# Kernel tuning notes

Hardware: AMD Instinct MI355X
Metric: run time of the kernel (lower is better)

Reference implementation:

```python
import jax, jax.numpy as jnp
import numpy as np

DIM = 768
H = 12  # num_heads -> head width W = 64 (required by internal reshapes)


def setup_inputs() -> dict:
    key = jax.random.key(0)
    ks = jax.random.split(key, 16)
    B, S = 1, 128  # V = Q = A = 128 tokens
    d = {
        "v": jax.random.normal(ks[0], (B, S, DIM), jnp.float32),
        "q": jax.random.normal(ks[1], (B, S, DIM), jnp.float32),
        "a": jax.random.normal(ks[2], (B, S, DIM), jnp.float32),
        "v_mask": jnp.ones((B, S), jnp.bool_),  # unused by the module, kept for signature parity
        "q_mask": jnp.ones((B, S), jnp.bool_),
        "a_mask": jnp.ones((B, S), jnp.bool_),
    }
    scale = 0.02
    names = ["Wv", "Wq", "Wa", "Wvo", "Wqo", "Wao"]
    for i, n in enumerate(names):
        d[n] = jax.random.normal(ks[3 + i], (DIM, DIM), jnp.float32) * scale
        d["b" + n[1:].lower()] = jnp.zeros((DIM,), jnp.float32)
    return d


def _heads(x):
    # (B, S, D) -> (B, H, S, W)
    B, S, D = x.shape
    return x.reshape(B, S, H, D // H).transpose(0, 2, 1, 3)


def reference(v, q, a, v_mask, q_mask, a_mask,
              Wv, bv, Wq, bq, Wa, ba, Wvo, bvo, Wqo, bqo, Wao, bao):
    B, Sv, D = v.shape
    Sq, Sa = q.shape[1], a.shape[1]
    W = D // H
    nv, nq, na = Sv // 8, Sq // 8, Sa // 8

    # first projections (masks are unused in the original forward)
    vp = v @ Wv + bv
    qp = q @ Wq + bq
    ap = a @ Wa + ba
    # output projections are applied to the ALREADY-projected tensors (as in source)
    vo = vp @ Wvo + bvo
    qo = qp @ Wqo + bqo
    ao = ap @ Wao + bao

    vh, qh, ah = _heads(vp), _heads(qp), _heads(ap)          # (B,H,S,W)
    voh, qoh, aoh = _heads(vo), _heads(qo), _heads(ao)

    # trilinear scores: (B,H,V,Q,A)
    att = jnp.einsum('bhvw,bhqw,bhaw->bhvqa', vh, qh, ah) / jnp.sqrt(jnp.asarray(W, vh.dtype))
    K = nv * nq * na
    # faithful to source: view(-1, H, nv*nq*na) then softmax over last axis, view back
    att = jax.nn.softmax(att.reshape(-1, H, K), axis=-1)
    att = att.reshape(-1, H, nv, nq, na)  # dropout p=0 -> identity
    B2 = att.shape[0]

    # source uses att.size(2) (= nv) for ALL three reshapes (requires V=Q=A)
    vor = voh.reshape(B2, H, nv, -1)
    qor = qoh.reshape(B2, H, nv, -1)
    aor = aoh.reshape(B2, H, nv, -1)

    v_out = jnp.einsum('bhvqa,bhvw->bvhw', att, vor).reshape(-1, DIM)
    q_out = jnp.einsum('bhvqa,bhqw->bqhw', att, qor).reshape(-1, DIM)
    a_out = jnp.einsum('bhvqa,bhaw->bahw', att, aor).reshape(-1, DIM)
    return (v_out, q_out, a_out)
```

## Files before the change

### kernel.cpp

```cpp
#include <hip/hip_runtime.h>


#define DIM   768
#define SEQ   128
#define NH    12
#define HW    64
#define PROJ_ELEMS (SEQ * DIM)
#define QOUT_OFF   98304
#define AOUT_OFF   196608

typedef _Float16 f16x8 __attribute__((ext_vector_type(8)));
typedef float    f32x4 __attribute__((ext_vector_type(4)));

__global__ __launch_bounds__(64) void proj_kernel(
    const void* __restrict__ A0, const void* __restrict__ A1, const void* __restrict__ A2,
    const float* __restrict__ W0, const float* __restrict__ W1, const float* __restrict__ W2,
    const float* __restrict__ b0, const float* __restrict__ b1, const float* __restrict__ b2,
    void* __restrict__ C0, void* __restrict__ C1, void* __restrict__ C2,
    int a_f16, int out_f16)
{
    const int mat = blockIdx.z;
    const void* __restrict__ A   = (mat == 0) ? A0 : (mat == 1) ? A1 : A2;
    const float* __restrict__ W  = (mat == 0) ? W0 : (mat == 1) ? W1 : W2;
    const float* __restrict__ bb = (mat == 0) ? b0 : (mat == 1) ? b1 : b2;
    void* __restrict__ C         = (mat == 0) ? C0 : (mat == 1) ? C1 : C2;

    const int m0   = blockIdx.x * 16;
    const int n0   = blockIdx.y * 16;
    const int lane = threadIdx.x & 63;
    const int fm   = lane & 15;
    const int fk   = (lane >> 4) << 3;

    const float* __restrict__ pw = W + fk * DIM + n0 + fm;

    f32x4 acc = (f32x4){0.f, 0.f, 0.f, 0.f};

    if (a_f16) {
        const _Float16* __restrict__ pa = (const _Float16*)A + (m0 + fm) * DIM + fk;
        #pragma unroll
        for (int s = 0; s < 24; ++s) {
            const f16x8 af = *(const f16x8*)(pa + 32 * s);
            const float* __restrict__ w = pw + 32 * s * DIM;
            float w0 = w[0 * DIM], w1 = w[1 * DIM], w2 = w[2 * DIM], w3 = w[3 * DIM];
            float w4 = w[4 * DIM], w5 = w[5 * DIM], w6 = w[6 * DIM], w7 = w[7 * DIM];
            f16x8 wf;
            wf[0] = (_Float16)w0; wf[1] = (_Float16)w1;
            wf[2] = (_Float16)w2; wf[3] = (_Float16)w3;
            wf[4] = (_Float16)w4; wf[5] = (_Float16)w5;
            wf[6] = (_Float16)w6; wf[7] = (_Float16)w7;
            acc = __builtin_amdgcn_mfma_f32_16x16x32_f16(af, wf, acc, 0, 0, 0);
        }
    } else {
        const float* __restrict__ pa = (const float*)A + (m0 + fm) * DIM + fk;
        #pragma unroll
        for (int s = 0; s < 24; ++s) {
            const f32x4 alo = *(const f32x4*)(pa + 32 * s);
            const f32x4 ahi = *(const f32x4*)(pa + 32 * s + 4);
            f16x8 af;
            af[0] = (_Float16)alo[0]; af[1] = (_Float16)alo[1];
            af[2] = (_Float16)alo[2]; af[3] = (_Float16)alo[3];
            af[4] = (_Float16)ahi[0]; af[5] = (_Float16)ahi[1];
            af[6] = (_Float16)ahi[2]; af[7] = (_Float16)ahi[3];
            const float* __restrict__ w = pw + 32 * s * DIM;
            float w0 = w[0 * DIM], w1 = w[1 * DIM], w2 = w[2 * DIM], w3 = w[3 * DIM];
            float w4 = w[4 * DIM], w5 = w[5 * DIM], w6 = w[6 * DIM], w7 = w[7 * DIM];
            f16x8 wf;
            wf[0] = (_Float16)w0; wf[1] = (_Float16)w1;
            wf[2] = (_Float16)w2; wf[3] = (_Float16)w3;
            wf[4] = (_Float16)w4; wf[5] = (_Float16)w5;
            wf[6] = (_Float16)w6; wf[7] = (_Float16)w7;
            acc = __builtin_amdgcn_mfma_f32_16x16x32_f16(af, wf, acc, 0, 0, 0);
        }
    }

    const int col  = n0 + fm;
    const int row0 = m0 + ((lane >> 4) << 2);
    const float bi = bb[col];
    #pragma unroll
    for (int rr = 0; rr < 4; ++rr) {
        const float val = acc[rr] + bi;
        if (out_f16) ((_Float16*)C)[(row0 + rr) * DIM + col] = (_Float16)val;
        else         ((float*)C)[(row0 + rr) * DIM + col]    = val;
    }
}

__global__ __launch_bounds__(256) void fused_attn_kernel(
    const _Float16* __restrict__ vpH, const _Float16* __restrict__ qpH,
    const _Float16* __restrict__ apH,
    const float* __restrict__ vo, const float* __restrict__ qo, const float* __restrict__ ao,
    float* __restrict__ out)
{
    const int vtok = blockIdx.x;
    const int h    = blockIdx.y;

    __shared__ _Float16 vqL[128][72];
    __shared__ _Float16 ahL[128][72];

    const int t    = threadIdx.x;
    const int w    = t >> 6;
    const int lane = t & 63;
    const int fm   = lane & 15;
    const int fk   = (lane >> 4) << 3;

    {
        const int r  = t >> 1;
        const int kh = (t & 1) << 5;
        const _Float16* pq = qpH + r    * DIM + h * HW + kh;
        const _Float16* pv = vpH + vtok * DIM + h * HW + kh;
        const _Float16* pa = apH + r    * DIM + h * HW + kh;
        #pragma unroll
        for (int u = 0; u < 4; ++u) {
            const f16x8 qv = *(const f16x8*)(pq + 8 * u);
            const f16x8 vv = *(const f16x8*)(pv + 8 * u);
            const f16x8 av = *(const f16x8*)(pa + 8 * u);
            *(f16x8*)&vqL[r][kh + 8 * u] = qv * vv;
            *(f16x8*)&ahL[r][kh + 8 * u] = av;
        }
    }
    __syncthreads();

    f32x4 acc[2][8];
    #pragma unroll
    for (int qt = 0; qt < 2; ++qt)
        #pragma unroll
        for (int at = 0; at < 8; ++at)
            acc[qt][at] = (f32x4){0.f, 0.f, 0.f, 0.f};

    const int q0 = 32 * w;
    #pragma unroll
    for (int ks = 0; ks < 2; ++ks) {
        const f16x8 af0 = *(const f16x8*)&vqL[q0 + fm     ][32 * ks + fk];
        const f16x8 af1 = *(const f16x8*)&vqL[q0 + 16 + fm][32 * ks + fk];
        #pragma unroll
        for (int at = 0; at < 8; ++at) {
            const f16x8 bf = *(const f16x8*)&ahL[16 * at + fm][32 * ks + fk];
            acc[0][at] = __builtin_amdgcn_mfma_f32_16x16x32_f16(af0, bf, acc[0][at], 0, 0, 0);
            acc[1][at] = __builtin_amdgcn_mfma_f32_16x16x32_f16(af1, bf, acc[1][at], 0, 0, 0);
        }
    }

    float sv[2][2] = {{0.f, 0.f}, {0.f, 0.f}};
    float sq[2][8];
    #pragma unroll
    for (int i = 0; i < 2; ++i)
        #pragma unroll
        for (int j = 0; j < 8; ++j) sq[i][j] = 0.f;
    float sa = 0.f;
    #pragma unroll
    for (int qt = 0; qt < 2; ++qt)
        #pragma unroll
        for (int at = 0; at < 8; ++at)
            #pragma unroll
            for (int rr = 0; rr < 4; ++rr) {
                const float e = __expf(acc[qt][at][rr] * 0.125f);
                sv[qt][rr >> 1] += e;
                sq[rr & 1][at]  += e;
                sa += e;
            }

    sa += __shfl_xor(sa, 16);
    sa += __shfl_xor(sa, 32);
    float tot = sa;
    tot += __shfl_xor(tot, 1);
    tot += __shfl_xor(tot, 2);
    tot += __shfl_xor(tot, 4);
    tot += __shfl_xor(tot, 8);
    const bool b0 = lane & 1;
    const bool b1 = lane & 2;
    float sF;
    {
        float snd0 = b0 ? sv[0][0] : sv[1][0];
        float snd1 = b0 ? sv[0][1] : sv[1][1];
        float r0 = __shfl_xor(snd0, 1);
        float r1 = __shfl_xor(snd1, 1);
        float s0 = (b0 ? sv[1][0] : sv[0][0]) + r0;
        float s1 = (b0 ? sv[1][1] : sv[0][1]) + r1;
        float snd = b1 ? s0 : s1;
        float r2 = __shfl_xor(snd, 2);
        sF = (b1 ? s1 : s0) + r2;
    }
    sF += __shfl_xor(sF, 4);
    sF += __shfl_xor(sF, 8);
    float s[16];
    #pragma unroll
    for (int i = 0; i < 2; ++i)
        #pragma unroll
        for (int j = 0; j < 8; ++j) s[i * 8 + j] = sq[i][j];
    #pragma unroll
    for (int k = 0; k < 4; ++k) {
        const int d = 1 << k;
        const int m = 16 >> (k + 1);
        const bool b = (lane >> k) & 1;
        #pragma unroll
        for (int x = 0; x < m; ++x) {
            const float snd = b ? s[x] : s[x + m];
            const float rcv = __shfl_xor(snd, d);
            s[x] = (b ? s[x + m] : s[x]) + rcv;
        }
    }
    s[0] += __shfl_xor(s[0], 16);
    s[0] += __shfl_xor(s[0], 32);

    const int g  = h * 512 + vtok * 4 + w;
    const int b2 = g / 12;
    const int h2 = g - b2 * 12;
    const float invZ = 1.0f / tot;
    const int obase = vtok * DIM + h * HW + w * 16;

    if (fm < 4) {
        const int quad = lane >> 4;
        const int bin  = (fm & 1) * 8 + quad * 2 + ((fm >> 1) & 1);
        out[(b2 * 16 + bin) * 12 + h2] = sF * invZ * vo[obase + bin];
    }
    if (lane < 16) {
        const int qbin = 8 * (lane & 1) + 4 * ((lane >> 1) & 1)
                       + 2 * ((lane >> 2) & 1) + (lane >> 3);
        out[QOUT_OFF + (b2 * 16 + qbin) * 12 + h2] = s[0] * invZ * qo[obase + qbin];
        out[AOUT_OFF + (b2 * 16 + lane) * 12 + h2] = sa   * invZ * ao[obase + lane];
    }
}

extern "C" void kernel_launch(void* const* d_in, const int* in_sizes, int n_in,
                              void* d_out, int out_size, void* d_ws, size_t ws_size,
                              hipStream_t stream)
{
    const float* v   = (const float*)d_in[0];
    const float* q   = (const float*)d_in[1];
    const float* a   = (const float*)d_in[2];
    const float* Wv  = (const float*)d_in[6];
    const float* bv  = (const float*)d_in[7];
    const float* Wq  = (const float*)d_in[8];
    const float* bq  = (const float*)d_in[9];
    const float* Wa  = (const float*)d_in[10];
    const float* ba  = (const float*)d_in[11];
    const float* Wvo = (const float*)d_in[12];
    const float* bvo = (const float*)d_in[13];
    const float* Wqo = (const float*)d_in[14];
    const float* bqo = (const float*)d_in[15];
    const float* Wao = (const float*)d_in[16];
    const float* bao = (const float*)d_in[17];

    float* out = (float*)d_out;

    _Float16* vpH = (_Float16*)d_ws;
    _Float16* qpH = vpH + PROJ_ELEMS;
    _Float16* apH = qpH + PROJ_ELEMS;
    float*    vo  = (float*)(apH + PROJ_ELEMS);
    float*    qo  = vo + PROJ_ELEMS;
    float*    ao  = qo + PROJ_ELEMS;

    proj_kernel<<<dim3(8, 48, 3), 64, 0, stream>>>(
        v, q, a, Wv, Wq, Wa,
        bv, bq, ba, vpH, qpH, apH, 0, 1);
    proj_kernel<<<dim3(8, 48, 3), 64, 0, stream>>>(
        vpH, qpH, apH, Wvo, Wqo, Wao,
        bvo, bqo, bao, vo, qo, ao, 1, 0);
    fused_attn_kernel<<<dim3(SEQ, NH), 256, 0, stream>>>(
        vpH, qpH, apH, vo, qo, ao, out);
}
```

Measured before the change: 144.0 us.

## Stage weight tile in shared memory as transposed f16 with XOR swizzle

The projection kernel no longer reads eight strided scalar fp32 weight values per MFMA step. It first loads the 768x16 weight slab with 16-byte vector loads, double-buffered in registers, converts it to f16 and writes it transposed into LDS using an XOR-swizzled layout. The MFMA loop then reads B fragments as single 16-byte LDS loads. This trades uncoalesced global gathers for a staging phase, a barrier and 24KB of LDS per 64-thread block, which may reduce occupancy.

```diff
diff --git a/kernel.cpp b/kernel.cpp
--- a/kernel.cpp
+++ b/kernel.cpp
@@ -29,26 +29,53 @@
     const int n0   = blockIdx.y * 16;
     const int lane = threadIdx.x & 63;
     const int fm   = lane & 15;
-    const int fk   = (lane >> 4) << 3;
-
-    const float* __restrict__ pw = W + fk * DIM + n0 + fm;
+    const int fkg  = lane >> 4;
+    const int fk   = fkg << 3;
+
+    __shared__ __align__(16) _Float16 T[16 * 768];
+
+    {
+        const int q = lane & 3;
+        const int g = lane >> 2;
+        const float* __restrict__ wp = W + (8 * g) * DIM + n0 + 4 * q;
+        f32x4 cur[8], nxt[8];
+        #pragma unroll
+        for (int i = 0; i < 8; ++i) cur[i] = *(const f32x4*)(wp + i * DIM);
+        #pragma unroll
+        for (int p = 0; p < 6; ++p) {
+            if (p < 5) {
+                const float* __restrict__ wn = wp + (p + 1) * 128 * DIM;
+                #pragma unroll
+                for (int i = 0; i < 8; ++i) nxt[i] = *(const f32x4*)(wn + i * DIM);
+            }
+            #pragma unroll
+            for (int j = 0; j < 4; ++j) {
+                f16x8 col;
+                #pragma unroll
+                for (int i = 0; i < 8; ++i) col[i] = (_Float16)cur[i][j];
+                const int n     = 4 * q + j;
+                const int chunk = (16 * p + g) ^ (n & 7);
+                *(f16x8*)&T[n * 768 + chunk * 8] = col;
+            }
+            if (p < 5) {
+                #pragma unroll
+                for (int i = 0; i < 8; ++i) cur[i] = nxt[i];
+            }
+        }
+    }
+    __syncthreads();
 
     f32x4 acc = (f32x4){0.f, 0.f, 0.f, 0.f};
+    const int rbase = fm * 768;
+    const int x7    = fm & 7;
 
     if (a_f16) {
         const _Float16* __restrict__ pa = (const _Float16*)A + (m0 + fm) * DIM + fk;
         #pragma unroll
         for (int s = 0; s < 24; ++s) {
             const f16x8 af = *(const f16x8*)(pa + 32 * s);
-            const float* __restrict__ w = pw + 32 * s * DIM;
-            float w0 = w[0 * DIM], w1 = w[1 * DIM], w2 = w[2 * DIM], w3 = w[3 * DIM];
-            float w4 = w[4 * DIM], w5 = w[5 * DIM], w6 = w[6 * DIM], w7 = w[7 * DIM];
-            f16x8 wf;
-            wf[0] = (_Float16)w0; wf[1] = (_Float16)w1;
-            wf[2] = (_Float16)w2; wf[3] = (_Float16)w3;
-            wf[4] = (_Float16)w4; wf[5] = (_Float16)w5;
-            wf[6] = (_Float16)w6; wf[7] = (_Float16)w7;
-            acc = __builtin_amdgcn_mfma_f32_16x16x32_f16(af, wf, acc, 0, 0, 0);
+            const f16x8 bf = *(const f16x8*)&T[rbase + (((4 * s + fkg) ^ x7) << 3)];
+            acc = __builtin_amdgcn_mfma_f32_16x16x32_f16(af, bf, acc, 0, 0, 0);
         }
     } else {
         const float* __restrict__ pa = (const float*)A + (m0 + fm) * DIM + fk;
@@ -61,15 +88,8 @@
             af[2] = (_Float16)alo[2]; af[3] = (_Float16)alo[3];
             af[4] = (_Float16)ahi[0]; af[5] = (_Float16)ahi[1];
             af[6] = (_Float16)ahi[2]; af[7] = (_Float16)ahi[3];
-            const float* __restrict__ w = pw + 32 * s * DIM;
-            float w0 = w[0 * DIM], w1 = w[1 * DIM], w2 = w[2 * DIM], w3 = w[3 * DIM];
-            float w4 = w[4 * DIM], w5 = w[5 * DIM], w6 = w[6 * DIM], w7 = w[7 * DIM];
-            f16x8 wf;
-            wf[0] = (_Float16)w0; wf[1] = (_Float16)w1;
-            wf[2] = (_Float16)w2; wf[3] = (_Float16)w3;
-            wf[4] = (_Float16)w4; wf[5] = (_Float16)w5;
-            wf[6] = (_Float16)w6; wf[7] = (_Float16)w7;
-            acc = __builtin_amdgcn_mfma_f32_16x16x32_f16(af, wf, acc, 0, 0, 0);
+            const f16x8 bf = *(const f16x8*)&T[rbase + (((4 * s + fkg) ^ x7) << 3)];
+            acc = __builtin_amdgcn_mfma_f32_16x16x32_f16(af, bf, acc, 0, 0, 0);
         }
     }
 
```

After: 148.9 us. +3.4%, slower.
